# Performance work log

Hardware: AMD Instinct MI355X
Metric: run time of the kernel (lower is better)

The kernel has to match this reference:

```python
import jax, jax.numpy as jnp
import numpy as np

B, D = 64, 1024
TAU = 1.0
NEG_SLOPE = 0.01  # torch LeakyReLU default


def setup_inputs() -> dict:
    key = jax.random.key(0)
    ks = jax.random.split(key, 7)
    lim = 1.0 / np.sqrt(D)
    return {
        "x": jax.random.normal(ks[0], (B, D), dtype=jnp.float32),
        "W1": jax.random.uniform(ks[1], (D, D), jnp.float32, -lim, lim),
        "b1": jax.random.uniform(ks[2], (D,), jnp.float32, -lim, lim),
        "W2": jax.random.uniform(ks[3], (D, D), jnp.float32, -lim, lim),
        "b2": jax.random.uniform(ks[4], (D,), jnp.float32, -lim, lim),
        "W3": jax.random.uniform(ks[5], (2, D), jnp.float32, -lim, lim),
        "b3": jax.random.uniform(ks[6], (2,), jnp.float32, -lim, lim),
    }


def _leaky(h):
    return jnp.where(h >= 0, h, NEG_SLOPE * h)


def _neural_sort(scores):
    # scores: [B, D]
    d = scores.shape[1]
    s = scores[..., None]                                  # [B, D, 1]
    A = jnp.abs(s - jnp.swapaxes(s, 1, 2))                 # [B, D, D] pairwise |s_i - s_j|
    # A @ (ones @ ones^T) == row-sum of A broadcast over columns
    Bsum = jnp.sum(A, axis=-1, keepdims=True)              # [B, D, 1]
    scaling = (d - 1 - 2 * jnp.arange(d)).astype(scores.dtype)  # (d+1-2*(i+1))
    C = s * scaling[None, None, :]                         # [B, D, D]
    P_max = jnp.swapaxes(C - Bsum, 1, 2)                   # [B, D, D]
    return jax.nn.softmax(P_max / TAU, axis=-1)


def reference(x, W1, b1, W2, b2, W3, b3):
    P_hat = _neural_sort(x)                                # [B, D, D]
    xs = jnp.einsum("bij,bj->bi", P_hat, x)                # soft-sorted x
    h = _leaky(xs @ W1.T + b1)
    h = _leaky(h @ W2.T + b2)
    return h @ W3.T + b3                                   # [B, 2]
```

## Files before the change

### kernel.cpp

```cpp
#include <hip/hip_runtime.h>
#include <math.h>

constexpr int Bn = 64;
constexpr int Dn = 1024;
constexpr float LOG2E = 1.4426950408889634f;
constexpr float LN2   = 0.6931471805599453f;

__device__ __forceinline__ float exp2_fast(float v) {
#if defined(__has_builtin)
#if __has_builtin(__builtin_amdgcn_exp2f)
  return __builtin_amdgcn_exp2f(v);
#else
  return exp2f(v);
#endif
#else
  return exp2f(v);
#endif
}

__global__ __launch_bounds__(256) void k_sortsoft(
    const float* __restrict__ x, float* __restrict__ xs_out,
    float* __restrict__ out) {
  __shared__ float  xs_[Dn];
  __shared__ float2 prs_[Dn];
  __shared__ int    bkt_[Dn];
  __shared__ float4 desc_[128];
  __shared__ int   cnt[64], base_[64], off_[64];
  __shared__ float Ssum[64], cN[64], cS[64];
  __shared__ float redM[4][64], redE[4][64], redD[4][64];

  int b   = blockIdx.x >> 4;
  int rc  = blockIdx.x & 15;
  int tid = threadIdx.x;

  if (tid < 64) { cnt[tid] = 0; off_[tid] = 0; Ssum[tid] = 0.f; }
  if (blockIdx.x == 0 && tid < 128) out[tid] = 0.f;
  __syncthreads();

  float4 v4 = *(const float4*)(x + b * Dn + tid * 4);
  float xv[4] = {v4.x, v4.y, v4.z, v4.w};
  int bk[4];
#pragma unroll
  for (int u = 0; u < 4; ++u) {
    float z = exp2_fast(-2.455532f * xv[u]);
    float p = 1.f / (1.f + z);
    int t = (int)(p * 64.f);
    bk[u] = t < 0 ? 0 : (t > 63 ? 63 : t);
    atomicAdd(&cnt[bk[u]], 1);
    atomicAdd(&Ssum[bk[u]], xv[u]);
  }
  __syncthreads();

  if (tid < 64) {
    int c = cnt[tid]; int si = c;
    float fs = Ssum[tid]; float ss = fs;
#pragma unroll
    for (int d = 1; d < 64; d <<= 1) {
      int oi = __shfl_up(si, d, 64);
      float os = __shfl_up(ss, d, 64);
      if (tid >= d) { si += oi; ss += os; }
    }
    base_[tid] = si - c;
    float Stot = __shfl(ss, 63, 64);
    float Slo = ss - fs;
    cN[tid] = (float)(2 * (si - c) + c - Dn);
    cS[tid] = Stot - 2.f * Slo - fs;
  }
  __syncthreads();

#pragma unroll
  for (int u = 0; u < 4; ++u) {
    int pos = base_[bk[u]] + atomicAdd(&off_[bk[u]], 1);
    xs_[pos] = xv[u];
    bkt_[pos] = bk[u];
  }
  __syncthreads();

#pragma unroll
  for (int r = 0; r < 4; ++r) {
    int p = r * 256 + tid;
    float xp = xs_[p];
    int q = bkt_[p];
    int lo = base_[q], hi = lo + cnt[q];
    float local = 0.f;
    for (int k = lo; k < hi; ++k) local += fabsf(xp - xs_[k]);
    float Bs = fmaf(xp, cN[q], cS[q]) + local;
    prs_[p] = make_float2(xp * LOG2E, -Bs * LOG2E);
  }
  __syncthreads();

  if (tid < 128) {
    int base = tid * 8;
    float xlo = xs_[base], xhi = xlo;
    int ilo = base, ihi = base;
#pragma unroll
    for (int k = 1; k < 8; ++k) {
      float xx = xs_[base + k];
      if (xx < xlo) { xlo = xx; ilo = base + k; }
      if (xx > xhi) { xhi = xx; ihi = base + k; }
    }
    float2 plo = prs_[ilo], phi = prs_[ihi];
    desc_[tid] = make_float4(plo.x, plo.y, phi.x, phi.y);
  }
  __syncthreads();

  int w = tid >> 6, lane = tid & 63;
  int i = rc * 64 + lane;
  float sc = (float)(Dn - 1 - 2 * i);
  float gm[32];
  float m = -3.4e38f;
#pragma unroll 8
  for (int q = 0; q < 32; ++q) {
    float4 d = desc_[q * 4 + w];
    float t0 = fmaf(sc, d.x, d.y);
    float t1 = fmaf(sc, d.z, d.w);
    float g = fmaxf(t0, t1);
    gm[q] = g;
    m = fmaxf(m, g);
  }
  redM[w][lane] = m;
  __syncthreads();
  float M = fmaxf(fmaxf(redM[0][lane], redM[1][lane]),
                  fmaxf(redM[2][lane], redM[3][lane]));
  float thresh = M - 32.f;

  float se = 0.f, sd = 0.f;
#pragma unroll 4
  for (int q = 0; q < 32; ++q) {
    if (__any(gm[q] > thresh)) {
      int base = (q * 4 + w) * 8;
#pragma unroll
      for (int u = 0; u < 8; ++u) {
        float2 v = prs_[base + u];
        float e = exp2_fast(fmaf(sc, v.x, v.y - M));
        se += e;
        sd = fmaf(e, v.x, sd);
      }
    }
  }
  redE[w][lane] = se;
  redD[w][lane] = sd;
  __syncthreads();
  if (tid < 64) {
    float SE = (redE[0][lane] + redE[1][lane]) + (redE[2][lane] + redE[3][lane]);
    float SD = (redD[0][lane] + redD[1][lane]) + (redD[2][lane] + redD[3][lane]);
    xs_out[b * Dn + rc * 64 + lane] = SD / SE * LN2;
  }
}

template <bool TAIL>
__global__ __launch_bounds__(256) void layer_kernel(
    const float* __restrict__ in, const float* __restrict__ W,
    const float* __restrict__ bias, float* __restrict__ out,
    const float* __restrict__ W3, const float* __restrict__ b3,
    float* __restrict__ out2) {
  __shared__ float s[8 * Dn];
  __shared__ float red2[4][8][9];
  __shared__ float r2[8][8][2];
  int xcd = blockIdx.x & 7;
  int idx = blockIdx.x >> 3;
  int nc = xcd * 16 + (idx & 15);
  int bc = idx >> 4;
  int tid = threadIdx.x;
  const float* src = in + bc * 8 * Dn;
#pragma unroll
  for (int u = 0; u < 8; ++u) {
    int gl = u * 256 + tid;
    int r = gl >> 8, g = gl & 255;
    int gs = g ^ ((g >> 3) & 7);
    *(float4*)&s[r * Dn + gs * 4] = *(const float4*)(src + gl * 4);
  }
  __syncthreads();

  int c  = tid & 7;
  int kc = tid >> 3;
  int w  = tid >> 6, lane = tid & 63;
  const float* wp = W + (size_t)(nc * 8 + c) * Dn + kc * 32;
  float acc[8] = {0.f, 0.f, 0.f, 0.f, 0.f, 0.f, 0.f, 0.f};
#pragma unroll
  for (int kq = 0; kq < 8; ++kq) {
    float4 wv = *(const float4*)(wp + kq * 4);
    int gs = kc * 8 + (kq ^ (kc & 7));
    const float* sp = s + gs * 4;
#pragma unroll
    for (int bl = 0; bl < 8; ++bl) {
      float4 av = *(const float4*)(sp + bl * Dn);
      acc[bl] = fmaf(av.x, wv.x, fmaf(av.y, wv.y,
                fmaf(av.z, wv.z, fmaf(av.w, wv.w, acc[bl]))));
    }
  }
#pragma unroll
  for (int bl = 0; bl < 8; ++bl) {
    float v = acc[bl];
    v += __shfl_xor(v, 8, 64);
    v += __shfl_xor(v, 16, 64);
    v += __shfl_xor(v, 32, 64);
    acc[bl] = v;
  }
  if (lane < 8) {
#pragma unroll
    for (int bl = 0; bl < 8; ++bl) red2[w][bl][lane] = acc[bl];
  }
  __syncthreads();

  if (!TAIL) {
    if (tid < 64) {
      int bl2 = tid >> 3, nl2 = tid & 7;
      int n2 = nc * 8 + nl2;
      float hs = (red2[0][bl2][nl2] + red2[1][bl2][nl2]) +
                 (red2[2][bl2][nl2] + red2[3][bl2][nl2]);
      float h = hs + bias[n2];
      h = h >= 0.f ? h : 0.01f * h;
      out[(bc * 8 + bl2) * Dn + n2] = h;
    }
  } else {
    if (tid < 64) {
      int bl2 = tid >> 3, nl2 = tid & 7;
      int n2 = nc * 8 + nl2;
      float hs = (red2[0][bl2][nl2] + red2[1][bl2][nl2]) +
                 (red2[2][bl2][nl2] + red2[3][bl2][nl2]);
      float h = hs + bias[n2];
      h = h >= 0.f ? h : 0.01f * h;
      r2[bl2][nl2][0] = h * W3[n2];
      r2[bl2][nl2][1] = h * W3[Dn + n2];
    }
    __syncthreads();
    if (tid < 16) {
      int bl2 = tid >> 1, o = tid & 1;
      float t = 0.f;
#pragma unroll
      for (int q = 0; q < 8; ++q) t += r2[bl2][q][o];
      if (nc == 0) t += b3[o];
      atomicAdd(out2 + (bc * 8 + bl2) * 2 + o, t);
    }
  }
}

extern "C" void kernel_launch(void* const* d_in, const int* in_sizes, int n_in,
                              void* d_out, int out_size, void* d_ws, size_t ws_size,
                              hipStream_t stream) {
  const float* x  = (const float*)d_in[0];
  const float* W1 = (const float*)d_in[1];
  const float* b1 = (const float*)d_in[2];
  const float* W2 = (const float*)d_in[3];
  const float* b2 = (const float*)d_in[4];
  const float* W3 = (const float*)d_in[5];
  const float* b3 = (const float*)d_in[6];
  float* out = (float*)d_out;
  float* ws = (float*)d_ws;

  float* xs = ws;
  float* h1 = xs + Bn * Dn;

  k_sortsoft<<<Bn * 16, 256, 0, stream>>>(x, xs, out);
  layer_kernel<false><<<1024, 256, 0, stream>>>(xs, W1, b1, h1,
                                                nullptr, nullptr, nullptr);
  layer_kernel<true><<<1024, 256, 0, stream>>>(h1, W2, b2, nullptr,
                                               W3, b3, out);
}
```

Before: 104.4 us.

## Give each wave two output columns over full K and reduce in-wave with butterfly shuffles

Each wave of the layer kernel now owns two output neurons across the whole K dimension, with each lane covering a 16-element K slice. Before, 8 neurons were spread across lanes and every wave saw only a quarter of K. Each activation float4 read from shared memory now feeds two weight vectors, and the cross-wave shared-memory reduction and its barrier are gone. Results are combined with a transpose-style butterfly shuffle reduction inside the wave. The cost is more registers and a different shared-memory bank access pattern for the swizzled activation reads.

```diff
diff --git a/kernel.cpp b/kernel.cpp
--- a/kernel.cpp
+++ b/kernel.cpp
@@ -155,7 +155,6 @@
     const float* __restrict__ W3, const float* __restrict__ b3,
     float* __restrict__ out2) {
   __shared__ float s[8 * Dn];
-  __shared__ float red2[4][8][9];
   __shared__ float r2[8][8][2];
   int xcd = blockIdx.x & 7;
   int idx = blockIdx.x >> 3;
@@ -172,66 +171,70 @@
   }
   __syncthreads();
 
-  int c  = tid & 7;
-  int kc = tid >> 3;
-  int w  = tid >> 6, lane = tid & 63;
-  const float* wp = W + (size_t)(nc * 8 + c) * Dn + kc * 32;
-  float acc[8] = {0.f, 0.f, 0.f, 0.f, 0.f, 0.f, 0.f, 0.f};
-#pragma unroll
-  for (int kq = 0; kq < 8; ++kq) {
-    float4 wv = *(const float4*)(wp + kq * 4);
-    int gs = kc * 8 + (kq ^ (kc & 7));
+  int c4   = tid >> 6;
+  int kc   = tid & 63;
+  int lane = tid & 63;
+  int n0 = nc * 8 + c4 * 2;
+  const float* w0 = W + (size_t)(n0 + 0) * Dn + kc * 16;
+  const float* w1 = W + (size_t)(n0 + 1) * Dn + kc * 16;
+  float acc0[8] = {0.f, 0.f, 0.f, 0.f, 0.f, 0.f, 0.f, 0.f};
+  float acc1[8] = {0.f, 0.f, 0.f, 0.f, 0.f, 0.f, 0.f, 0.f};
+#pragma unroll
+  for (int j = 0; j < 4; ++j) {
+    float4 wv0 = *(const float4*)(w0 + j * 4);
+    float4 wv1 = *(const float4*)(w1 + j * 4);
+    int g = kc * 4 + j;
+    int gs = g ^ ((g >> 3) & 7);
     const float* sp = s + gs * 4;
 #pragma unroll
     for (int bl = 0; bl < 8; ++bl) {
       float4 av = *(const float4*)(sp + bl * Dn);
-      acc[bl] = fmaf(av.x, wv.x, fmaf(av.y, wv.y,
-                fmaf(av.z, wv.z, fmaf(av.w, wv.w, acc[bl]))));
-    }
-  }
-#pragma unroll
-  for (int bl = 0; bl < 8; ++bl) {
-    float v = acc[bl];
-    v += __shfl_xor(v, 8, 64);
-    v += __shfl_xor(v, 16, 64);
-    v += __shfl_xor(v, 32, 64);
-    acc[bl] = v;
-  }
-  if (lane < 8) {
-#pragma unroll
-    for (int bl = 0; bl < 8; ++bl) red2[w][bl][lane] = acc[bl];
-  }
-  __syncthreads();
-
-  if (!TAIL) {
-    if (tid < 64) {
-      int bl2 = tid >> 3, nl2 = tid & 7;
-      int n2 = nc * 8 + nl2;
-      float hs = (red2[0][bl2][nl2] + red2[1][bl2][nl2]) +
-                 (red2[2][bl2][nl2] + red2[3][bl2][nl2]);
-      float h = hs + bias[n2];
-      h = h >= 0.f ? h : 0.01f * h;
+      acc0[bl] = fmaf(av.x, wv0.x, fmaf(av.y, wv0.y,
+                 fmaf(av.z, wv0.z, fmaf(av.w, wv0.w, acc0[bl]))));
+      acc1[bl] = fmaf(av.x, wv1.x, fmaf(av.y, wv1.y,
+                 fmaf(av.z, wv1.z, fmaf(av.w, wv1.w, acc1[bl]))));
+    }
+  }
+
+  float v[16];
+#pragma unroll
+  for (int bl = 0; bl < 8; ++bl) { v[2 * bl] = acc0[bl]; v[2 * bl + 1] = acc1[bl]; }
+#pragma unroll
+  for (int bit = 0; bit < 4; ++bit) {
+    int d = 1 << bit;
+    bool hi = (lane & d) != 0;
+#pragma unroll
+    for (int i = 0; i < (8 >> bit); ++i) {
+      float keep = hi ? v[2 * i + 1] : v[2 * i];
+      float send = hi ? v[2 * i] : v[2 * i + 1];
+      v[i] = keep + __shfl_xor(send, d, 64);
+    }
+  }
+  float t = v[0];
+  t += __shfl_xor(t, 16, 64);
+  t += __shfl_xor(t, 32, 64);
+
+  if (lane < 16) {
+    int bl2 = lane >> 1, cl = lane & 1;
+    int n2 = n0 + cl;
+    float h = t + bias[n2];
+    h = h >= 0.f ? h : 0.01f * h;
+    if (!TAIL) {
       out[(bc * 8 + bl2) * Dn + n2] = h;
-    }
-  } else {
-    if (tid < 64) {
-      int bl2 = tid >> 3, nl2 = tid & 7;
-      int n2 = nc * 8 + nl2;
-      float hs = (red2[0][bl2][nl2] + red2[1][bl2][nl2]) +
-                 (red2[2][bl2][nl2] + red2[3][bl2][nl2]);
-      float h = hs + bias[n2];
-      h = h >= 0.f ? h : 0.01f * h;
-      r2[bl2][nl2][0] = h * W3[n2];
-      r2[bl2][nl2][1] = h * W3[Dn + n2];
-    }
+    } else {
+      r2[bl2][c4 * 2 + cl][0] = h * W3[n2];
+      r2[bl2][c4 * 2 + cl][1] = h * W3[Dn + n2];
+    }
+  }
+  if (TAIL) {
     __syncthreads();
     if (tid < 16) {
       int bl2 = tid >> 1, o = tid & 1;
-      float t = 0.f;
-#pragma unroll
-      for (int q = 0; q < 8; ++q) t += r2[bl2][q][o];
-      if (nc == 0) t += b3[o];
-      atomicAdd(out2 + (bc * 8 + bl2) * 2 + o, t);
+      float tt = 0.f;
+#pragma unroll
+      for (int q = 0; q < 8; ++q) tt += r2[bl2][q][o];
+      if (nc == 0) tt += b3[o];
+      atomicAdd(out2 + (bc * 8 + bl2) * 2 + o, tt);
     }
   }
 }
```

Result: faster. 101.9 us (-2.4%).
